# Performance work log

Hardware: AMD Instinct MI355X
Metric: run time of the kernel (lower is better)

Reference implementation:

```python
import jax, jax.numpy as jnp
import numpy as np

N_NODES = 50000
N_EDGES = 1600000
GL = [512, 256, 16]
LL = [16, 16]


def setup_inputs() -> dict:
    key = jax.random.key(0)
    ks = jax.random.split(key, 10)
    H = jax.random.normal(ks[0], (N_NODES, GL[0]), dtype=jnp.float32)
    edge_index = jax.random.randint(ks[1], (2, N_EDGES), 0, N_NODES, dtype=jnp.int64)
    edge_vals = jax.random.uniform(ks[2], (N_EDGES,), dtype=jnp.float32)
    def uni(k, shape, fan_out):
        stdv = 1.0 / np.sqrt(fan_out)
        return jax.random.uniform(k, shape, minval=-stdv, maxval=stdv, dtype=jnp.float32)
    W1 = uni(ks[3], (GL[0], GL[1]), GL[1])
    b1 = uni(ks[4], (GL[1],), GL[1])
    W2 = uni(ks[5], (GL[1], GL[2]), GL[2])
    b2 = uni(ks[6], (GL[2],), GL[2])
    Wl = uni(ks[7], (LL[0], LL[1]), LL[0])
    bl = uni(ks[8], (LL[1],), LL[0])
    return {"H": H, "edge_index": edge_index, "edge_vals": edge_vals,
            "W1": W1, "b1": b1, "W2": W2, "b2": b2, "Wl": Wl, "bl": bl}


def reference(H, edge_index, edge_vals, W1, b1, W2, b2, Wl, bl):
    row, col = edge_index[0], edge_index[1]
    n = H.shape[0]

    def spmm(X):  # (A @ X) for sparse COO A, X: [N, d]
        return jax.ops.segment_sum(edge_vals[:, None] * X[col], row, num_segments=n)

    # graph conv layers (dropout condition idx < len-2 never fires with 2 layers)
    H1 = jax.nn.relu(spmm(H @ W1) + b1)
    H2 = jax.nn.relu(spmm(H1 @ W2) + b2)
    # linear head
    H3 = jax.nn.relu(H2 @ Wl + bl)
    Y = jax.nn.softmax(H3, axis=1)  # [N, g]

    # NCut loss: sum_e w_e * dot(Y[row_e]/Gamma, (1-Y)[col_e])
    D = jax.ops.segment_sum(edge_vals, row, num_segments=n)  # degree [N]
    Gamma = Y.T @ D  # [g]
    YbyG = Y / Gamma[None, :]
    loss = jnp.sum(jnp.sum(YbyG[row] * (1.0 - Y)[col], axis=1) * edge_vals)
    return jnp.reshape(loss, (1,))
```

## Files before the change

kernel.cpp:

```cpp
#include <hip/hip_runtime.h>


constexpr int NN = 50000;
constexpr int NE = 1600000;
constexpr int F0 = 512;
constexpr int F1 = 256;
constexpr int G  = 16;
constexpr int CB   = 196;
constexpr int CCAP = 10240;
constexpr int CHUNK = 4096;
constexpr int NPASS = 391;
constexpr int ECH = 1024;

typedef short  s16x8 __attribute__((ext_vector_type(8)));
typedef float  f32x4 __attribute__((ext_vector_type(4)));
typedef float  f32x2 __attribute__((ext_vector_type(2)));
typedef int    i32x4 __attribute__((ext_vector_type(4)));
typedef int    i32x2 __attribute__((ext_vector_type(2)));
typedef float  fv4   __attribute__((ext_vector_type(4)));

static __device__ __forceinline__ unsigned short f2bf(float f) {
    union { float f; unsigned u; } v; v.f = f;
    unsigned r = (v.u + 0x7FFFu + ((v.u >> 16) & 1u)) >> 16;
    return (unsigned short)r;
}
static __device__ __forceinline__ float bf2f(unsigned short u) {
    union { unsigned u; float f; } v; v.u = (unsigned)u << 16;
    return v.f;
}

static __device__ __forceinline__ void glds16(const void* g, void* l) {
    __builtin_amdgcn_global_load_lds(
        (const __attribute__((address_space(1))) unsigned int*)g,
        (__attribute__((address_space(3))) unsigned int*)l,
        16, 0, 0);
}

static __device__ __forceinline__ s16x8 pack8(f32x4 a, f32x4 b) {
    union { unsigned u[4]; s16x8 v; } r;
    asm("v_cvt_pk_bf16_f32 %0, %1, %2" : "=v"(r.u[0]) : "v"(a.x), "v"(a.y));
    asm("v_cvt_pk_bf16_f32 %0, %1, %2" : "=v"(r.u[1]) : "v"(a.z), "v"(a.w));
    asm("v_cvt_pk_bf16_f32 %0, %1, %2" : "=v"(r.u[2]) : "v"(b.x), "v"(b.y));
    asm("v_cvt_pk_bf16_f32 %0, %1, %2" : "=v"(r.u[3]) : "v"(b.z), "v"(b.w));
    return r.v;
}

__global__ __launch_bounds__(256) void k_castW1(const float* __restrict__ W1, unsigned short* __restrict__ W1t) {
    int idx = blockIdx.x * 256 + threadIdx.x;
    if (idx < F0 * F1) {
        int k = idx >> 8, n = idx & 255;
        W1t[n * F0 + k] = f2bf(W1[idx]);
    }
}

__global__ __launch_bounds__(256) void k_fused1(const float* __restrict__ H,
                                                const unsigned short* __restrict__ W1t,
                                                unsigned char* __restrict__ XW,
                                                const int* __restrict__ row, const int* __restrict__ col,
                                                const float* __restrict__ ev,
                                                int* __restrict__ ccur, int2* __restrict__ cbuf) {
    __shared__ __align__(16) unsigned char smem[49152];
    const int bid = blockIdx.x;
    const int tid = threadIdx.x;
    const int stripe = bid / 3;
    const int pos = bid - stripe * 3;

    if (pos != 1) {
        const int gidx = stripe * 2 + (pos >> 1);
        const int lane = tid & 63;
        const int wave = tid >> 6;
        const int bm = (gidx >> 1) * 128;
        const int bn = (gidx & 1) * 128;
        const int m_off = (wave & 1) * 64;
        const int n_off = (wave >> 1) * 64;
        const int l15  = lane & 15;
        const int quad = lane >> 4;

        f32x4 acc[4][4];
#pragma unroll
        for (int i = 0; i < 4; ++i)
#pragma unroll
            for (int j = 0; j < 4; ++j) acc[i][j] = (f32x4)0.f;

        const int arow16 = tid >> 4;
        const int slA    = (tid & 15) ^ (arow16 & 7);
        const int browB  = tid >> 3;
        const int slB    = (tid & 7) ^ (browB & 7);
        const int wvB    = wave * 1024;

#define STAGE(K0)                                                              \
        do {                                                                   \
            _Pragma("unroll")                                                  \
            for (int p = 0; p < 8; ++p) {                                      \
                int gr = bm + p * 16 + arow16;                                 \
                gr = gr < NN ? gr : NN - 1;                                    \
                glds16(&H[(size_t)gr * F0 + (K0) + slA * 4],                   \
                       smem + p * 4096 + wvB);                                 \
            }                                                                  \
            _Pragma("unroll")                                                  \
            for (int p = 0; p < 4; ++p)                                        \
                glds16(&W1t[(size_t)(bn + p * 32 + browB) * F0 + (K0) + slB * 8], \
                       smem + 32768 + p * 4096 + wvB);                         \
        } while (0)

        STAGE(0);
        asm volatile("s_waitcnt vmcnt(0)" ::: "memory");
        __syncthreads();
        for (int k0 = 0; k0 < F0; k0 += 64) {
#pragma unroll
            for (int kk6 = 0; kk6 < 2; ++kk6) {
                const int kk = kk6 * 32;
                s16x8 af[4], bfr[4];
#pragma unroll
                for (int mi = 0; mi < 4; ++mi) {
                    const int r = m_off + mi * 16 + l15;
                    const int sw = r & 7;
                    const int s0 = (kk >> 2) + quad * 2;
                    const char* rb = (const char*)smem + r * 256;
                    f32x4 v0 = *(const f32x4*)(rb + (((s0    ) ^ sw) << 4));
                    f32x4 v1 = *(const f32x4*)(rb + (((s0 + 1) ^ sw) << 4));
                    af[mi] = pack8(v0, v1);
                }
#pragma unroll
                for (int ni = 0; ni < 4; ++ni) {
                    const int r = n_off + ni * 16 + l15;
                    const int sb = (kk >> 3) + quad;
                    bfr[ni] = *(const s16x8*)((const char*)smem + 32768 + r * 128
                                              + ((sb ^ (r & 7)) << 4));
                }
#pragma unroll
                for (int mi = 0; mi < 4; ++mi)
#pragma unroll
                    for (int ni = 0; ni < 4; ++ni)
                        acc[mi][ni] = __builtin_amdgcn_mfma_f32_16x16x32_bf16(af[mi], bfr[ni], acc[mi][ni], 0, 0, 0);
            }
            __syncthreads();
            if (k0 + 64 < F0) {
                STAGE(k0 + 64);
                asm volatile("s_waitcnt vmcnt(0)" ::: "memory");
            }
            __syncthreads();
        }
#undef STAGE
#pragma unroll
        for (int mi = 0; mi < 4; ++mi) {
            int r0 = bm + m_off + mi * 16 + quad * 4;
#pragma unroll
            for (int reg = 0; reg < 4; ++reg) {
                int gr = r0 + reg;
                if (gr < NN) {
                    unsigned char* orow = &XW[(size_t)gr * F1 + bn + n_off];
#pragma unroll
                    for (int ni = 0; ni < 4; ++ni) {
                        int pk = __builtin_amdgcn_cvt_pk_fp8_f32(acc[mi][ni][reg], 0.f, 0, false);
                        orow[ni * 16 + l15] = (unsigned char)(pk & 0xff);
                    }
                }
            }
        }
    } else {
        int* hcnt  = (int*)smem;
        int* hbase = hcnt + CB;
        for (int i = tid; i < CB; i += 256) hcnt[i] = 0;
        __syncthreads();

        const int base4 = stripe * (CHUNK / 4);
        int recx[16]; float recw[16]; int cb[16];
#pragma unroll
        for (int k = 0; k < 4; ++k) {
            int i4 = base4 + k * 256 + tid;
            bool ok = i4 < NE / 4;
            i32x4 r = ok ? __builtin_nontemporal_load(&((const i32x4*)row)[i4]) : (i32x4)0;
            i32x4 c = ok ? __builtin_nontemporal_load(&((const i32x4*)col)[i4]) : (i32x4)0;
            fv4   w = ok ? __builtin_nontemporal_load(&((const fv4*)ev)[i4])   : (fv4)0.f;
            int rr[4] = {r.x, r.y, r.z, r.w};
            int cc[4] = {c.x, c.y, c.z, c.w};
            float ww[4] = {w.x, w.y, w.z, w.w};
#pragma unroll
            for (int j = 0; j < 4; ++j) {
                int slot = k * 4 + j;
                if (ok) {
                    cb[slot] = rr[j] >> 8;
                    atomicAdd(&hcnt[cb[slot]], 1);
                } else {
                    cb[slot] = -1;
                }
                recx[slot] = (cc[j] << 16) | (rr[j] & 255);
                recw[slot] = ww[j];
            }
        }
        __syncthreads();
        for (int i = tid; i < CB; i += 256) {
            int cnt = hcnt[i];
            hbase[i] = (cnt > 0) ? atomicAdd(&ccur[i], cnt) : 0;
            hcnt[i] = 0;
        }
        __syncthreads();
#pragma unroll
        for (int slot = 0; slot < 16; ++slot) {
            if (cb[slot] >= 0) {
                int p = hbase[cb[slot]] + atomicAdd(&hcnt[cb[slot]], 1);
                cbuf[(size_t)cb[slot] * CCAP + p] = make_int2(recx[slot], __float_as_int(recw[slot]));
            }
        }
    }
}

__global__ __launch_bounds__(256) void k_passB(const int2* __restrict__ cbuf, const int* __restrict__ ccur,
                                               int* __restrict__ rowptr, int2* __restrict__ E) {
    __shared__ int cnt[256];
    __shared__ int scn[256];
    __shared__ int red[4];
    const int cbk = blockIdx.x;
    const int tid = threadIdx.x;
    cnt[tid] = 0;

    int b = 0;
    for (int i = tid; i < cbk; i += 256) b += ccur[i];
#pragma unroll
    for (int off = 1; off < 64; off <<= 1) b += __shfl_xor(b, off, 64);
    if ((tid & 63) == 0) red[tid >> 6] = b;
    __syncthreads();
    const int base = red[0] + red[1] + red[2] + red[3];

    const int total = ccur[cbk];
    const int2* src = cbuf + (size_t)cbk * CCAP;
    for (int i = tid; i < total; i += 256) atomicAdd(&cnt[src[i].x & 255], 1);
    __syncthreads();

    scn[tid] = cnt[tid];
    __syncthreads();
    for (int off = 1; off < 256; off <<= 1) {
        int t = (tid >= off) ? scn[tid - off] : 0;
        __syncthreads();
        scn[tid] += t;
        __syncthreads();
    }
    const int excl = scn[tid] - cnt[tid];
    const int r = (cbk << 8) + tid;
    if (r <= NN) rowptr[r] = base + excl;
    __syncthreads();
    cnt[tid] = base + excl;
    __syncthreads();
    for (int i = tid; i < total; i += 256) {
        int2 rec = src[i];
        int rl = rec.x & 255;
        int c  = (int)((unsigned)rec.x >> 16);
        int p = atomicAdd(&cnt[rl], 1);
        E[p] = make_int2(c << 8, rec.y);
    }
}

__global__ __launch_bounds__(256) void k_spmm1(const unsigned char* __restrict__ XW, const int* __restrict__ rowptr,
                                               const int2* __restrict__ E,
                                               const float* __restrict__ b1, const float* __restrict__ W2,
                                               unsigned short* __restrict__ Z, float* __restrict__ Dv) {
    __shared__ float W2P[G * 320];
    __shared__ i32x2 Esh[ECH];
    const int tid = threadIdx.x;
#pragma unroll
    for (int it = 0; it < 16; ++it) {
        int elem = it * 256 + tid;
        int j = elem >> 8;
        int l = (elem >> 4) & 15;
        int t = elem & 15;
        W2P[j * 320 + l * 20 + t] = W2[(l * 16 + t) * 16 + j];
    }
    const int lane16 = tid & 15;
    const int loff = lane16 * 16;
    const int n = blockIdx.x * 16 + (tid >> 4);
    const int nb0 = rowptr[blockIdx.x * 16];
    const int nb1 = rowptr[blockIdx.x * 16 + 16];
    const int s = rowptr[n];
    const int e = rowptr[n + 1];
    const i32x2* E2 = (const i32x2*)E;

    f32x2 acc2[8];
#pragma unroll
    for (int q = 0; q < 8; ++q) acc2[q] = (f32x2)0.f;
    float wsum = 0.f;

#define GATH8(GG, WW, BASE)                                        \
        _Pragma("unroll")                                          \
        for (int k = 0; k < 8; ++k) {                              \
            i32x2 ed = Esh[(BASE) - w0 + k];                       \
            WW[k] = __int_as_float(ed.y);                          \
            GG[k] = *(const uint4*)(XW + ed.x + loff);             \
        }
#define COMP8(GG, WW)                                              \
        _Pragma("unroll")                                          \
        for (int k = 0; k < 8; ++k) {                              \
            const unsigned gw[4] = {GG[k].x, GG[k].y, GG[k].z, GG[k].w}; \
            f32x2 wp; wp.x = WW[k]; wp.y = WW[k];                  \
            _Pragma("unroll")                                      \
            for (int q = 0; q < 4; ++q) {                          \
                f32x2 lo = __builtin_amdgcn_cvt_pk_f32_fp8(gw[q], false); \
                f32x2 hi = __builtin_amdgcn_cvt_pk_f32_fp8(gw[q], true);  \
                acc2[2 * q]     = __builtin_elementwise_fma(lo, wp, acc2[2 * q]);     \
                acc2[2 * q + 1] = __builtin_elementwise_fma(hi, wp, acc2[2 * q + 1]); \
            }                                                      \
            wsum += WW[k];                                         \
        }

    for (int w0 = nb0; w0 < nb1; w0 += ECH) {
        const int wend = (w0 + ECH < nb1) ? (w0 + ECH) : nb1;
        __syncthreads();
        for (int t = tid; t < wend - w0; t += 256)
            Esh[t] = __builtin_nontemporal_load(&E2[w0 + t]);
        __syncthreads();

        const int gs = (s > w0) ? s : w0;
        const int ge = (e < wend) ? e : wend;

        uint4 ggA[8], ggB[8];
        float wA[8], wB[8];
        int i = gs;
        if (i + 8 <= ge) { GATH8(ggA, wA, i) }
        while (i + 24 <= ge) {
            GATH8(ggB, wB, i + 8)
            COMP8(ggA, wA)
            GATH8(ggA, wA, i + 16)
            COMP8(ggB, wB)
            i += 16;
        }
        if (i + 16 <= ge) {
            GATH8(ggB, wB, i + 8)
            COMP8(ggA, wA)
            COMP8(ggB, wB)
            i += 16;
        } else if (i + 8 <= ge) {
            COMP8(ggA, wA)
            i += 8;
        }
        for (; i < ge; i += 4) {
            int of4[4]; float w4v[4];
#pragma unroll
            for (int k = 0; k < 4; ++k) {
                int idx = i + k;
                bool ok = idx < ge;
                i32x2 ed = Esh[(ok ? idx : gs) - w0];
                of4[k] = ed.x; w4v[k] = ok ? __int_as_float(ed.y) : 0.f;
            }
            uint4 gg[4];
#pragma unroll
            for (int k = 0; k < 4; ++k)
                gg[k] = *(const uint4*)(XW + of4[k] + loff);
#pragma unroll
            for (int k = 0; k < 4; ++k) {
                const unsigned gw[4] = {gg[k].x, gg[k].y, gg[k].z, gg[k].w};
                f32x2 wp; wp.x = w4v[k]; wp.y = w4v[k];
#pragma unroll
                for (int q = 0; q < 4; ++q) {
                    f32x2 lo = __builtin_amdgcn_cvt_pk_f32_fp8(gw[q], false);
                    f32x2 hi = __builtin_amdgcn_cvt_pk_f32_fp8(gw[q], true);
                    acc2[2 * q]     = __builtin_elementwise_fma(lo, wp, acc2[2 * q]);
                    acc2[2 * q + 1] = __builtin_elementwise_fma(hi, wp, acc2[2 * q + 1]);
                }
                wsum += w4v[k];
            }
        }
    }
#undef GATH8
#undef COMP8

    if (lane16 == 0) Dv[n] = wsum;

#pragma unroll
    for (int q = 0; q < 4; ++q) {
        float4 bb = *(const float4*)&b1[loff + q * 4];
        acc2[2 * q].x     = fmaxf(acc2[2 * q].x     + bb.x, 0.f);
        acc2[2 * q].y     = fmaxf(acc2[2 * q].y     + bb.y, 0.f);
        acc2[2 * q + 1].x = fmaxf(acc2[2 * q + 1].x + bb.z, 0.f);
        acc2[2 * q + 1].y = fmaxf(acc2[2 * q + 1].y + bb.w, 0.f);
    }

    float p[G];
#pragma unroll
    for (int j = 0; j < G; ++j) {
        float pj = 0.f;
#pragma unroll
        for (int q = 0; q < 4; ++q) {
            float4 w4 = *(const float4*)&W2P[j * 320 + lane16 * 20 + q * 4];
            pj += acc2[2 * q].x * w4.x + acc2[2 * q].y * w4.y
                + acc2[2 * q + 1].x * w4.z + acc2[2 * q + 1].y * w4.w;
        }
        p[j] = pj;
    }
#pragma unroll
    for (int off = 1; off < 16; off <<= 1) {
#pragma unroll
        for (int j = 0; j < G; ++j) p[j] += __shfl_xor(p[j], off, 64);
    }
    if (lane16 == 0) {
        unsigned zp[8];
#pragma unroll
        for (int j = 0; j < 8; ++j)
            zp[j] = (unsigned)f2bf(p[2 * j]) | ((unsigned)f2bf(p[2 * j + 1]) << 16);
        uint4* zo = (uint4*)&Z[n * G];
        zo[0] = make_uint4(zp[0], zp[1], zp[2], zp[3]);
        zo[1] = make_uint4(zp[4], zp[5], zp[6], zp[7]);
    }
}

__global__ __launch_bounds__(256) void k_head(const unsigned short* __restrict__ Zb, const int* __restrict__ rowptr,
                                              const int2* __restrict__ E,
                                              const float* __restrict__ b2, const float* __restrict__ Wl,
                                              const float* __restrict__ bl, const float* __restrict__ Dv,
                                              unsigned short* __restrict__ Yb, float* __restrict__ GammaP) {
    __shared__ float WlS[G * G];
    __shared__ float gsh[G];
    const int tid = threadIdx.x;
    if (tid < G * G) WlS[tid] = Wl[tid];
    if (tid < G) gsh[tid] = 0.f;
    __syncthreads();
    const int lane = tid & 63;
    const int g = lane >> 3;
    const int d = lane & 7;
    const int n = blockIdx.x * 4 + (tid >> 6);
    const int s = __builtin_amdgcn_readfirstlane(rowptr[n]);
    const int e = __builtin_amdgcn_readfirstlane(rowptr[n + 1]);
    const char* Zc = (const char*)Zb;
    const i32x2* Ev = (const i32x2*)E;

    float a0 = 0.f, a1 = 0.f;
    for (int base = s; base < e; base += 16) {
        int i0 = base + g;
        int i1 = base + 8 + g;
        i32x2 e0 = __builtin_nontemporal_load(&Ev[(i0 < e) ? i0 : s]);
        i32x2 e1 = __builtin_nontemporal_load(&Ev[(i1 < e) ? i1 : s]);
        float w0 = (i0 < e) ? __int_as_float(e0.y) : 0.f;
        float w1 = (i1 < e) ? __int_as_float(e1.y) : 0.f;
        unsigned z0 = *(const unsigned*)(Zc + (e0.x >> 3) + d * 4);
        unsigned z1 = *(const unsigned*)(Zc + (e1.x >> 3) + d * 4);
        a0 = fmaf(w0, bf2f((unsigned short)(z0 & 0xffff)), a0);
        a1 = fmaf(w0, bf2f((unsigned short)(z0 >> 16)), a1);
        a0 = fmaf(w1, bf2f((unsigned short)(z1 & 0xffff)), a0);
        a1 = fmaf(w1, bf2f((unsigned short)(z1 >> 16)), a1);
    }
    a0 += __shfl_xor(a0, 8, 64);  a1 += __shfl_xor(a1, 8, 64);
    a0 += __shfl_xor(a0, 16, 64); a1 += __shfl_xor(a1, 16, 64);
    a0 += __shfl_xor(a0, 32, 64); a1 += __shfl_xor(a1, 32, 64);

    const int j = lane & 15;
    float e0v = __shfl(a0, j >> 1, 64);
    float e1v = __shfl(a1, j >> 1, 64);
    float accj = (j & 1) ? e1v : e0v;

    float h2 = fmaxf(accj + b2[j], 0.f);
    float s3 = 0.f;
#pragma unroll
    for (int k = 0; k < G; ++k) s3 = fmaf(__shfl(h2, k, 64), WlS[k * G + j], s3);
    float h3 = fmaxf(s3 + bl[j], 0.f);
    float m = h3;
    m = fmaxf(m, __shfl_xor(m, 1, 64));
    m = fmaxf(m, __shfl_xor(m, 2, 64));
    m = fmaxf(m, __shfl_xor(m, 4, 64));
    m = fmaxf(m, __shfl_xor(m, 8, 64));
    float ex = __expf(h3 - m);
    float se = ex;
    se += __shfl_xor(se, 1, 64);
    se += __shfl_xor(se, 2, 64);
    se += __shfl_xor(se, 4, 64);
    se += __shfl_xor(se, 8, 64);
    float y = ex / se;
    if (lane < G) {
        Yb[n * G + j] = f2bf(y);
        atomicAdd(&gsh[j], y * Dv[n]);
    }
    __syncthreads();
    if (tid < G) atomicAdd(&GammaP[(blockIdx.x & 63) * G + tid], gsh[tid]);
}

__global__ __launch_bounds__(256) void k_loss(const unsigned short* __restrict__ Yb, const int* __restrict__ rowptr,
                                              const int2* __restrict__ E, float* __restrict__ SjP) {
    __shared__ float sjsh[G];
    const int tid = threadIdx.x;
    if (tid < G) sjsh[tid] = 0.f;
    __syncthreads();
    const int lane = tid & 63;
    const int g = lane >> 3;
    const int d = lane & 7;
    const int n = blockIdx.x * 4 + (tid >> 6);
    const int s = __builtin_amdgcn_readfirstlane(rowptr[n]);
    const int e = __builtin_amdgcn_readfirstlane(rowptr[n + 1]);
    const char* Yc = (const char*)Yb;
    const i32x2* Ev = (const i32x2*)E;

    unsigned yr = *(const unsigned*)(Yc + ((size_t)n << 5) + d * 4);
    float y0 = bf2f((unsigned short)(yr & 0xffff));
    float y1 = bf2f((unsigned short)(yr >> 16));

    float s0 = 0.f, s1 = 0.f;
    for (int base = s; base < e; base += 16) {
        int i0 = base + g;
        int i1 = base + 8 + g;
        i32x2 e0 = __builtin_nontemporal_load(&Ev[(i0 < e) ? i0 : s]);
        i32x2 e1 = __builtin_nontemporal_load(&Ev[(i1 < e) ? i1 : s]);
        float w0 = (i0 < e) ? __int_as_float(e0.y) : 0.f;
        float w1 = (i1 < e) ? __int_as_float(e1.y) : 0.f;
        unsigned z0 = *(const unsigned*)(Yc + (e0.x >> 3) + d * 4);
        unsigned z1 = *(const unsigned*)(Yc + (e1.x >> 3) + d * 4);
        s0 = fmaf(w0 * y0, bf2f((unsigned short)(z0 & 0xffff)), s0);
        s1 = fmaf(w0 * y1, bf2f((unsigned short)(z0 >> 16)), s1);
        s0 = fmaf(w1 * y0, bf2f((unsigned short)(z1 & 0xffff)), s0);
        s1 = fmaf(w1 * y1, bf2f((unsigned short)(z1 >> 16)), s1);
    }
    s0 += __shfl_xor(s0, 8, 64);  s1 += __shfl_xor(s1, 8, 64);
    s0 += __shfl_xor(s0, 16, 64); s1 += __shfl_xor(s1, 16, 64);
    s0 += __shfl_xor(s0, 32, 64); s1 += __shfl_xor(s1, 32, 64);
    if (lane < 8) {
        atomicAdd(&sjsh[2 * lane],     s0);
        atomicAdd(&sjsh[2 * lane + 1], s1);
    }
    __syncthreads();
    if (tid < G) atomicAdd(&SjP[(blockIdx.x & 63) * G + tid], sjsh[tid]);
}

__global__ void k_final(const float* __restrict__ GammaP, const float* __restrict__ SjP,
                        float* __restrict__ out) {
    const int tid = threadIdx.x;
    const int j = tid & 15;
    float gam = 0.f, sj = 0.f;
    for (int b = 0; b < 64; ++b) {
        gam += GammaP[b * G + j];
        sj  += SjP[b * G + j];
    }
    float v = sj / gam;
    v += __shfl_xor(v, 1, 64);
    v += __shfl_xor(v, 2, 64);
    v += __shfl_xor(v, 4, 64);
    v += __shfl_xor(v, 8, 64);
    if (tid == 0) out[0] = 16.0f - v;
}

static inline size_t alignup(size_t x) { return (x + 255) & ~(size_t)255; }

extern "C" void kernel_launch(void* const* d_in, const int* in_sizes, int n_in,
                              void* d_out, int out_size, void* d_ws, size_t ws_size,
                              hipStream_t stream) {
    const float* H  = (const float*)d_in[0];
    const int*   ei = (const int*)d_in[1];
    const float* ev = (const float*)d_in[2];
    const float* W1 = (const float*)d_in[3];
    const float* b1 = (const float*)d_in[4];
    const float* W2 = (const float*)d_in[5];
    const float* b2 = (const float*)d_in[6];
    const float* Wl = (const float*)d_in[7];
    const float* bl = (const float*)d_in[8];
    const int* row = ei;
    const int* col = ei + NE;

    char* base = (char*)d_ws;
    size_t off = 0;
    unsigned char*  XW  = (unsigned char*)(base + off);  off = alignup(off + (size_t)NN * F1);
    unsigned short* W1t = (unsigned short*)(base + off); off = alignup(off + (size_t)F0 * F1 * 2);
    unsigned short* Z   = (unsigned short*)(base + off); off = alignup(off + (size_t)NN * G * 2);
    unsigned short* Yb  = (unsigned short*)(base + off); off = alignup(off + (size_t)NN * G * 2);
    float* Dv     = (float*)(base + off); off = alignup(off + (size_t)NN * 4);
    size_t zoff = off;
    int*   ccur   = (int*)(base + off);   off += (size_t)CB * 4;
    float* GammaP = (float*)(base + off); off += (size_t)64 * G * 4;
    float* SjP    = (float*)(base + off); off += (size_t)64 * G * 4;
    size_t zsize = off - zoff;
    off = alignup(off);
    int*   rowptr = (int*)(base + off);   off = alignup(off + (size_t)(NN + 1) * 4);
    int2*  cbuf   = (int2*)(base + off);  off = alignup(off + (size_t)CB * CCAP * 8);
    int2*  E      = (int2*)(base + off);  off = alignup(off + (size_t)NE * 8);

    hipMemsetAsync(base + zoff, 0, zsize, stream);

    k_castW1<<<dim3((F0 * F1 + 255) / 256), dim3(256), 0, stream>>>(W1, W1t);
    k_fused1<<<dim3(3 * NPASS), dim3(256), 0, stream>>>(
        H, W1t, XW, row, col, ev, ccur, cbuf);
    k_passB<<<dim3(CB), dim3(256), 0, stream>>>(cbuf, ccur, rowptr, E);
    k_spmm1<<<dim3(NN / 16), dim3(256), 0, stream>>>(XW, rowptr, E, b1, W2, Z, Dv);
    k_head<<<dim3(NN / 4), dim3(256), 0, stream>>>(Z, rowptr, E, b2, Wl, bl, Dv, Yb, GammaP);
    k_loss<<<dim3(NN / 4), dim3(256), 0, stream>>>(Yb, rowptr, E, SjP);
    k_final<<<dim3(1), dim3(64), 0, stream>>>(GammaP, SjP, (float*)d_out);
}
```

Baseline: 354.4 us.

## Double-buffer GEMM shared-memory staging to overlap loads with MFMA compute

Replaces the single-buffered K=64 staging loop in the fused XW GEMM with a two-buffer K=32 pipeline. Each step prefetches the next slice into the alternate buffer before computing on the current one, and waits with a partial vmcnt so global-to-LDS copies overlap with MFMA work. The swizzle patterns change to fit the narrower K slice. In exchange there are more iterations and barriers, with the same LDS footprint and shared-memory occupancy.

```diff
diff --git a/kernel.cpp b/kernel.cpp
--- a/kernel.cpp
+++ b/kernel.cpp
@@ -11,6 +11,7 @@
 constexpr int CHUNK = 4096;
 constexpr int NPASS = 391;
 constexpr int ECH = 1024;
+constexpr int BUFB = 24576;
 
 typedef short  s16x8 __attribute__((ext_vector_type(8)));
 typedef float  f32x4 __attribute__((ext_vector_type(4)));
@@ -59,7 +60,7 @@
                                                 const int* __restrict__ row, const int* __restrict__ col,
                                                 const float* __restrict__ ev,
                                                 int* __restrict__ ccur, int2* __restrict__ cbuf) {
-    __shared__ __align__(16) unsigned char smem[49152];
+    __shared__ __align__(16) unsigned char smem[2 * BUFB];
     const int bid = blockIdx.x;
     const int tid = threadIdx.x;
     const int stripe = bid / 3;
@@ -82,66 +83,73 @@
 #pragma unroll
             for (int j = 0; j < 4; ++j) acc[i][j] = (f32x4)0.f;
 
-        const int arow16 = tid >> 4;
-        const int slA    = (tid & 15) ^ (arow16 & 7);
-        const int browB  = tid >> 3;
-        const int slB    = (tid & 7) ^ (browB & 7);
-        const int wvB    = wave * 1024;
-
-#define STAGE(K0)                                                              \
+        const int rowA = tid >> 3;
+        const int slA  = (tid & 7) ^ ((tid >> 3) & 7);
+        const int rowB = tid >> 2;
+        const int slB  = (tid & 3) ^ ((tid >> 3) & 3);
+        const int wv   = wave * 1024;
+
+#define STAGE(K0, BOF)                                                         \
         do {                                                                   \
             _Pragma("unroll")                                                  \
-            for (int p = 0; p < 8; ++p) {                                      \
-                int gr = bm + p * 16 + arow16;                                 \
+            for (int p = 0; p < 4; ++p) {                                      \
+                int gr = bm + p * 32 + rowA;                                   \
                 gr = gr < NN ? gr : NN - 1;                                    \
                 glds16(&H[(size_t)gr * F0 + (K0) + slA * 4],                   \
-                       smem + p * 4096 + wvB);                                 \
+                       smem + (BOF) + p * 4096 + wv);                          \
             }                                                                  \
             _Pragma("unroll")                                                  \
-            for (int p = 0; p < 4; ++p)                                        \
-                glds16(&W1t[(size_t)(bn + p * 32 + browB) * F0 + (K0) + slB * 8], \
-                       smem + 32768 + p * 4096 + wvB);                         \
+            for (int p = 0; p < 2; ++p)                                        \
+                glds16(&W1t[(size_t)(bn + p * 64 + rowB) * F0 + (K0) + slB * 8], \
+                       smem + (BOF) + 16384 + p * 4096 + wv);                  \
         } while (0)
 
-        STAGE(0);
+#define COMPUTE(BOF)                                                           \
+        do {                                                                   \
+            const char* Ab = (const char*)smem + (BOF);                        \
+            const char* Bb = (const char*)smem + (BOF) + 16384;                \
+            s16x8 af[4], bfr[4];                                               \
+            _Pragma("unroll")                                                  \
+            for (int mi = 0; mi < 4; ++mi) {                                   \
+                const int r = m_off + mi * 16 + l15;                           \
+                const int sw = r & 7;                                          \
+                const int s0 = quad * 2;                                       \
+                const char* rb = Ab + r * 128;                                 \
+                f32x4 v0 = *(const f32x4*)(rb + (((s0    ) ^ sw) << 4));       \
+                f32x4 v1 = *(const f32x4*)(rb + (((s0 + 1) ^ sw) << 4));       \
+                af[mi] = pack8(v0, v1);                                        \
+            }                                                                  \
+            _Pragma("unroll")                                                  \
+            for (int ni = 0; ni < 4; ++ni) {                                   \
+                const int r = n_off + ni * 16 + l15;                           \
+                bfr[ni] = *(const s16x8*)(Bb + r * 64                          \
+                                          + ((quad ^ ((r >> 1) & 3)) << 4));   \
+            }                                                                  \
+            _Pragma("unroll")                                                  \
+            for (int mi = 0; mi < 4; ++mi)                                     \
+                _Pragma("unroll")                                              \
+                for (int ni = 0; ni < 4; ++ni)                                 \
+                    acc[mi][ni] = __builtin_amdgcn_mfma_f32_16x16x32_bf16(af[mi], bfr[ni], acc[mi][ni], 0, 0, 0); \
+        } while (0)
+
+        STAGE(0, 0);
+        int cur = 0;
+        for (int t = 0; t < 15; ++t) {
+            STAGE((t + 1) * 32, (cur ^ 1) * BUFB);
+            asm volatile("s_waitcnt vmcnt(6)" ::: "memory");
+            __builtin_amdgcn_s_barrier();
+            asm volatile("" ::: "memory");
+            COMPUTE(cur * BUFB);
+            asm volatile("" ::: "memory");
+            __builtin_amdgcn_s_barrier();
+            cur ^= 1;
+        }
         asm volatile("s_waitcnt vmcnt(0)" ::: "memory");
-        __syncthreads();
-        for (int k0 = 0; k0 < F0; k0 += 64) {
-#pragma unroll
-            for (int kk6 = 0; kk6 < 2; ++kk6) {
-                const int kk = kk6 * 32;
-                s16x8 af[4], bfr[4];
-#pragma unroll
-                for (int mi = 0; mi < 4; ++mi) {
-                    const int r = m_off + mi * 16 + l15;
-                    const int sw = r & 7;
-                    const int s0 = (kk >> 2) + quad * 2;
-                    const char* rb = (const char*)smem + r * 256;
-                    f32x4 v0 = *(const f32x4*)(rb + (((s0    ) ^ sw) << 4));
-                    f32x4 v1 = *(const f32x4*)(rb + (((s0 + 1) ^ sw) << 4));
-                    af[mi] = pack8(v0, v1);
-                }
-#pragma unroll
-                for (int ni = 0; ni < 4; ++ni) {
-                    const int r = n_off + ni * 16 + l15;
-                    const int sb = (kk >> 3) + quad;
-                    bfr[ni] = *(const s16x8*)((const char*)smem + 32768 + r * 128
-                                              + ((sb ^ (r & 7)) << 4));
-                }
-#pragma unroll
-                for (int mi = 0; mi < 4; ++mi)
-#pragma unroll
-                    for (int ni = 0; ni < 4; ++ni)
-                        acc[mi][ni] = __builtin_amdgcn_mfma_f32_16x16x32_bf16(af[mi], bfr[ni], acc[mi][ni], 0, 0, 0);
-            }
-            __syncthreads();
-            if (k0 + 64 < F0) {
-                STAGE(k0 + 64);
-                asm volatile("s_waitcnt vmcnt(0)" ::: "memory");
-            }
-            __syncthreads();
-        }
+        __builtin_amdgcn_s_barrier();
+        asm volatile("" ::: "memory");
+        COMPUTE(cur * BUFB);
 #undef STAGE
+#undef COMPUTE
 #pragma unroll
         for (int mi = 0; mi < 4; ++mi) {
             int r0 = bm + m_off + mi * 16 + quad * 4;
```

New measurement: 357.3 us. Within noise of the previous version (+0.8%).
